# Kernel tuning notes

Measured on AMD Instinct MI355X. Metric: run time of the kernel, lower is better.

The kernel has to match this reference:

```python
import jax, jax.numpy as jnp
import numpy as np

D_MODEL = 1024
NUM_HEADS = 16
DFF = 4096
LN_EPS = 1e-08
CLIP = 10.0


def setup_inputs() -> dict:
    key = jax.random.key(0)
    ks = jax.random.split(key, 12)
    d, h, f = D_MODEL, NUM_HEADS, DFF
    s = 1.0 / np.sqrt(d)
    inp = {
        "x": jax.random.normal(ks[0], (4, 2048, d), dtype=jnp.float32),
        "wq": jax.random.normal(ks[1], (d, d), dtype=jnp.float32) * s,
        "bq": jnp.zeros((d,), jnp.float32),
        "wk": jax.random.normal(ks[2], (d, d), dtype=jnp.float32) * s,
        "bk": jnp.zeros((d,), jnp.float32),
        "wv": jax.random.normal(ks[3], (d, d), dtype=jnp.float32) * s,
        "bv": jnp.zeros((d,), jnp.float32),
        "wo": jax.random.normal(ks[4], (d, d), dtype=jnp.float32) * s,
        "bo": jnp.zeros((d,), jnp.float32),
        "w1": jax.random.normal(ks[5], (d, f), dtype=jnp.float32) * s,
        "b1": jnp.zeros((f,), jnp.float32),
        "w2": jax.random.normal(ks[6], (f, d), dtype=jnp.float32) * (1.0 / np.sqrt(f)),
        "b2": jnp.zeros((d,), jnp.float32),
        "ln_gamma": jnp.ones((d,), jnp.float32),
        "ln_beta": jnp.zeros((d,), jnp.float32),
    }
    return inp


def layernorm(x, gamma, beta):
    mu = jnp.mean(x, axis=-1, keepdims=True)
    var = jnp.var(x, axis=-1, keepdims=True)
    return (x - mu) * jax.lax.rsqrt(var + LN_EPS) * gamma + beta


def encoder_layer(x, wq, bq, wk, bk, wv, bv, wo, bo, w1, b1, w2, b2, ln_gamma, ln_beta):
    B, S, d = x.shape
    H = NUM_HEADS
    Dh = d // H
    q = (x @ wq + bq).reshape(B, S, H, Dh).transpose(0, 2, 1, 3)  # bhsd
    k = (x @ wk + bk).reshape(B, S, H, Dh).transpose(0, 2, 1, 3)
    v = (x @ wv + bv).reshape(B, S, H, Dh).transpose(0, 2, 1, 3)
    logits = jnp.einsum('bhqd,bhkd->bhqk', q, k) / jnp.sqrt(jnp.float32(Dh))
    logits = jnp.clip(logits, -CLIP, CLIP)
    attn = jax.nn.softmax(logits, axis=-1)
    ctx = jnp.einsum('bhqk,bhkd->bhqd', attn, v)
    ctx = ctx.transpose(0, 2, 1, 3).reshape(B, S, d)
    attn_out = ctx @ wo + bo
    out1 = layernorm(x + attn_out, ln_gamma, ln_beta)
    ffn = jax.nn.relu(out1 @ w1 + b1) @ w2 + b2
    return layernorm(out1 + ffn, ln_gamma, ln_beta)


def reference(x, wq, bq, wk, bk, wv, bv, wo, bo, w1, b1, w2, b2, ln_gamma, ln_beta):
    return encoder_layer(x, wq, bq, wk, bk, wv, bv, wo, bo, w1, b1, w2, b2, ln_gamma, ln_beta)
```

## Files before the change

### kernel.cpp

```cpp
#include <hip/hip_runtime.h>
#include <stdint.h>

#define D_MODEL 1024
#define NHEAD 16
#define DH 64
#define DFF 4096
#define BATCH 4
#define SEQ 2048
#define MTOT (BATCH*SEQ)

#define QSCALE 0.18033688011112043f
#define CLIP2  14.426950408889634f

typedef short short8 __attribute__((ext_vector_type(8)));
typedef float f32x4 __attribute__((ext_vector_type(4)));
typedef unsigned int uint;

__device__ inline unsigned short f2bf(float f) {
  union { float f; unsigned u; } v; v.f = f;
  unsigned r = v.u + 0x7fffu + ((v.u >> 16) & 1u);
  return (unsigned short)(r >> 16);
}
__device__ inline float bf2f(unsigned short b) {
  union { unsigned u; float f; } v; v.u = ((unsigned)b) << 16;
  return v.f;
}
__device__ inline unsigned pack_trunc(float lo, float hi) {
  union { float f; unsigned u; } a, b; a.f = lo; b.f = hi;
  return __builtin_amdgcn_perm(b.u, a.u, 0x07060302u);
}
__device__ __forceinline__ void async16(const unsigned short* g, unsigned short* l) {
  __builtin_amdgcn_global_load_lds(
      (const __attribute__((address_space(1))) unsigned int*)g,
      (__attribute__((address_space(3))) unsigned int*)l, 16, 0, 0);
}

__global__ void cast_kernel(const float* __restrict__ in, unsigned short* __restrict__ out, int n4) {
  int i = blockIdx.x * blockDim.x + threadIdx.x;
  if (i < n4) {
    float4 v = ((const float4*)in)[i];
    ushort4 o;
    o.x = f2bf(v.x); o.y = f2bf(v.y); o.z = f2bf(v.z); o.w = f2bf(v.w);
    ((ushort4*)out)[i] = o;
  }
}

__global__ void transpose_weights_kernel(
    const float* __restrict__ wq, const float* __restrict__ wk,
    const float* __restrict__ wv, const float* __restrict__ wo,
    const float* __restrict__ w1, const float* __restrict__ w2,
    unsigned short* __restrict__ wqkvT, unsigned short* __restrict__ woT,
    unsigned short* __restrict__ w1T, unsigned short* __restrict__ w2T) {
  __shared__ unsigned short tile[32][33];
  const int id = blockIdx.x;
  const float* in; unsigned short* out; int K, N, n0, k0; float scale = 1.0f;
  if (id < 4096) {
    const int wi = id >> 10, t = id & 1023;
    switch (wi) {
      case 0:  in = wq; out = wqkvT;           scale = QSCALE; break;
      case 1:  in = wk; out = wqkvT + 1048576; break;
      case 2:  in = wv; out = wqkvT + 2097152; break;
      default: in = wo; out = woT;             break;
    }
    K = 1024; N = 1024; n0 = (t & 31) * 32; k0 = (t >> 5) * 32;
  } else if (id < 8192) {
    const int t = id - 4096;
    in = w1; out = w1T; K = 1024; N = 4096; n0 = (t & 127) * 32; k0 = (t >> 7) * 32;
  } else {
    const int t = id - 8192;
    in = w2; out = w2T; K = 4096; N = 1024; n0 = (t & 31) * 32; k0 = (t >> 5) * 32;
  }
  const int tx = threadIdx.x & 31, ty = threadIdx.x >> 5;
#pragma unroll
  for (int j = 0; j < 32; j += 8)
    tile[ty + j][tx] = f2bf(in[(size_t)(k0 + ty + j) * N + n0 + tx] * scale);
  __syncthreads();
#pragma unroll
  for (int j = 0; j < 32; j += 8)
    out[(size_t)(n0 + ty + j) * K + k0 + tx] = tile[tx][ty + j];
}

__global__ void bias_concat_kernel(const float* __restrict__ bq, const float* __restrict__ bk,
                                   const float* __restrict__ bv, float* __restrict__ o) {
  int i = blockIdx.x * 256 + threadIdx.x;
  if (i < 3 * D_MODEL) {
    float v = (i < D_MODEL) ? bq[i] * QSCALE
            : (i < 2 * D_MODEL) ? bk[i - D_MODEL] : bv[i - 2 * D_MODEL];
    o[i] = v;
  }
}

__global__ void transpose_v_kernel(const unsigned short* __restrict__ QKV,
                                   unsigned short* __restrict__ Vt) {
  __shared__ unsigned short tile[32][33];
  int bh = blockIdx.z, b = bh >> 4, h = bh & 15;
  int kv0 = blockIdx.x * 32, dh0 = blockIdx.y * 32;
  int tx = threadIdx.x & 31, ty = threadIdx.x >> 5;
#pragma unroll
  for (int j = 0; j < 32; j += 8)
    tile[ty + j][tx] = QKV[(size_t)(b * SEQ + kv0 + ty + j) * 3072 + 2048 + h * DH + dh0 + tx];
  __syncthreads();
#pragma unroll
  for (int j = 0; j < 32; j += 8)
    Vt[(size_t)(bh * DH + dh0 + ty + j) * SEQ + kv0 + tx] = tile[tx][ty + j];
}

template<int RELU, int OUT_BF16, int KSPLIT, int BIAS>
__global__ __launch_bounds__(256, 4) void gemm_bt_kernel(
    const unsigned short* __restrict__ A,
    const unsigned short* __restrict__ Bt,
    const float* __restrict__ bias,
    void* __restrict__ Cout,
    int M, int N, int K) {
  __shared__ __align__(16) unsigned short As[128][32];
  __shared__ __align__(16) unsigned short Bs[128][32];
  const int GX = N >> 7;
  const int xcd = blockIdx.x & 7;
  int li = blockIdx.x >> 3;
  int kh = 0;
  if (KSPLIT == 2) { kh = li & 1; li >>= 1; }
  const int im = xcd * 8 + li / GX;
  const int in_ = li % GX;
  const int m0 = im * 128, n0 = in_ * 128;
  const int tid = threadIdx.x;
  const int wave = tid >> 6, lane = tid & 63;
  const int wm = (wave >> 1) * 64, wn = (wave & 1) * 64;
  const int lm = lane & 15, lq = lane >> 4, lk = (lane >> 4) * 8;
  const int sr = tid >> 2;
  const int sc = (tid & 3) * 8;
  f32x4 acc[4][4] = {};

  const int kbeg = (KSPLIT == 2) ? kh * (K >> 1) : 0;
  const int kend = (KSPLIT == 2) ? kbeg + (K >> 1) : K;
  for (int k0 = kbeg; k0 < kend; k0 += 32) {
    __syncthreads();
#pragma unroll
    for (int s = 0; s < 2; s++) {
      int row = sr + s * 64;
      async16(A  + (size_t)(m0 + row) * K + k0 + sc, &As[0][0] + row * 32 + sc);
      async16(Bt + (size_t)(n0 + row) * K + k0 + sc, &Bs[0][0] + row * 32 + sc);
    }
    __syncthreads();
    short8 af[4], bfr[4];
#pragma unroll
    for (int t = 0; t < 4; t++) {
      af[t]  = *(const short8*)(&As[wm + t * 16 + lm][lk]);
      bfr[t] = *(const short8*)(&Bs[wn + t * 16 + lm][lk]);
    }
#pragma unroll
    for (int mt = 0; mt < 4; mt++)
#pragma unroll
      for (int nt = 0; nt < 4; nt++)
        acc[mt][nt] = __builtin_amdgcn_mfma_f32_16x16x32_bf16(af[mt], bfr[nt], acc[mt][nt], 0, 0, 0);
  }
  unsigned short* Cb = (unsigned short*)Cout + (KSPLIT == 2 ? (size_t)kh * M * N : 0);
#pragma unroll
  for (int nt = 0; nt < 4; nt++) {
    int col = n0 + wn + nt * 16 + lm;
    float bv = BIAS ? bias[col] : 0.0f;
#pragma unroll
    for (int mt = 0; mt < 4; mt++) {
#pragma unroll
      for (int r = 0; r < 4; r++) {
        int row = m0 + wm + mt * 16 + lq * 4 + r;
        float v = acc[mt][nt][r] + bv;
        if (RELU) v = fmaxf(v, 0.0f);
        if (OUT_BF16) Cb[(size_t)row * N + col] = f2bf(v);
        else          ((float*)Cout)[(size_t)row * N + col] = v;
      }
    }
  }
}

#define MFMA_Q(mh, nh)                                                                     \
  _Pragma("unroll")                                                                        \
  for (int ks = 0; ks < 2; ks++) {                                                         \
    _Pragma("unroll")                                                                      \
    for (int i = 0; i < 4; i++) {                                                          \
      _Pragma("unroll")                                                                    \
      for (int nn = 0; nn < 2; nn++) {                                                     \
        acc[(mh)*4 + i][(nh)*2 + nn] = __builtin_amdgcn_mfma_f32_16x16x32_bf16(            \
            af[i][ks], bf[(nh)*2 + nn][ks], acc[(mh)*4 + i][(nh)*2 + nn], 0, 0, 0);        \
      }                                                                                    \
    }                                                                                      \
  }

template<int RELU, int OUT_BF16, int KSPLIT, int BIAS>
__global__ __launch_bounds__(512, 2) void gemm256_bt_kernel(
    const unsigned short* __restrict__ A,
    const unsigned short* __restrict__ Bt,
    const float* __restrict__ bias,
    void* __restrict__ Cout,
    int M, int N, int K) {
  __shared__ __align__(16) unsigned short lds[65536];

  const int nwg = gridDim.x;
  int nid = (blockIdx.x & 7) * (nwg >> 3) + (blockIdx.x >> 3);
  int kh = 0;
  if (KSPLIT == 2) { kh = nid & 1; nid >>= 1; }
  const int GX = N >> 8;
  const int im = nid / GX, in_ = nid % GX;
  const int m0 = im * 256, n0 = in_ * 256;

  const int tid = threadIdx.x;
  const int lane = tid & 63, wave = tid >> 6;
  const int wm = (wave >> 2) * 128, wn = (wave & 3) * 64;
  const int lm = lane & 15, lg = lane >> 4;
  const int rot = lm & 7;
  const int aoff0 = ((lg) ^ rot) << 3;
  const int aoff1 = ((4 + lg) ^ rot) << 3;
  const int arow = (wm + lm) << 6;
  const int brow = (wn + lm) << 6;

  const int kbeg = (KSPLIT == 2) ? kh * (K >> 1) : 0;
  const int nk = ((KSPLIT == 2) ? (K >> 1) : K) >> 6;

  const int rb = tid >> 3;
  const int gcol = (((tid & 7) ^ (rb & 7)) << 3);
  const unsigned short* gA = A  + (size_t)(m0 + rb) * K + kbeg + gcol;
  const unsigned short* gB = Bt + (size_t)(n0 + rb) * K + kbeg + gcol;

  auto stage = [&](const unsigned short* g, int b, int st, unsigned short* seg) {
    async16(g + (size_t)b * 64 * K + (size_t)st * 64, seg + b * 4096 + tid * 8);
  };

  f32x4 acc[8][4] = {};

  {
    unsigned short* A0s = lds;
    unsigned short* B0s = lds + 16384;
    unsigned short* A1s = lds + 32768;
    unsigned short* B1s = lds + 49152;
    stage(gA, 0, 0, A0s); stage(gA, 2, 0, A0s);
    stage(gB, 0, 0, B0s); stage(gB, 1, 0, B0s);
    stage(gA, 1, 0, A0s); stage(gA, 3, 0, A0s);
    stage(gB, 2, 0, B0s); stage(gB, 3, 0, B0s);
    stage(gA, 0, 1, A1s); stage(gA, 2, 1, A1s);
    stage(gB, 0, 1, B1s); stage(gB, 1, 1, B1s);
    stage(gA, 1, 1, A1s); stage(gA, 3, 1, A1s);
    __builtin_amdgcn_s_waitcnt(0x0F76);
    __builtin_amdgcn_s_barrier();
  }

  for (int t = 0; t < nk; ++t) {
    const int cur = t & 1;
    unsigned short* LA = lds + (cur << 15);
    unsigned short* LB = LA + 16384;
    unsigned short* NA = lds + ((cur ^ 1) << 15);
    unsigned short* NB = NA + 16384;
    short8 af[4][2], bf[4][2];

    if (t + 1 < nk) { stage(gB, 2, t + 1, NB); stage(gB, 3, t + 1, NB); }
#pragma unroll
    for (int i = 0; i < 4; i++) {
      af[i][0] = *(const short8*)(LA + arow + i * 1024 + aoff0);
      af[i][1] = *(const short8*)(LA + arow + i * 1024 + aoff1);
    }
#pragma unroll
    for (int n = 0; n < 2; n++) {
      bf[n][0] = *(const short8*)(LB + brow + n * 1024 + aoff0);
      bf[n][1] = *(const short8*)(LB + brow + n * 1024 + aoff1);
    }
    __builtin_amdgcn_s_barrier();
    __builtin_amdgcn_s_setprio(1);
    MFMA_Q(0, 0);
    __builtin_amdgcn_s_setprio(0);
    __builtin_amdgcn_s_barrier();

    if (t + 2 < nk) { stage(gA, 0, t + 2, LA); stage(gA, 2, t + 2, LA); }
#pragma unroll
    for (int n = 2; n < 4; n++) {
      bf[n][0] = *(const short8*)(LB + brow + n * 1024 + aoff0);
      bf[n][1] = *(const short8*)(LB + brow + n * 1024 + aoff1);
    }
    __builtin_amdgcn_s_barrier();
    __builtin_amdgcn_s_setprio(1);
    MFMA_Q(0, 1);
    __builtin_amdgcn_s_setprio(0);
    __builtin_amdgcn_s_barrier();

    if (t + 2 < nk) { stage(gB, 0, t + 2, LB); stage(gB, 1, t + 2, LB); }
#pragma unroll
    for (int i = 0; i < 4; i++) {
      af[i][0] = *(const short8*)(LA + arow + 4096 + i * 1024 + aoff0);
      af[i][1] = *(const short8*)(LA + arow + 4096 + i * 1024 + aoff1);
    }
    __builtin_amdgcn_s_barrier();
    __builtin_amdgcn_s_setprio(1);
    MFMA_Q(1, 1);
    __builtin_amdgcn_s_setprio(0);
    __builtin_amdgcn_s_barrier();

    if (t + 2 < nk) {
      stage(gA, 1, t + 2, LA); stage(gA, 3, t + 2, LA);
      __builtin_amdgcn_s_waitcnt(0x0F76);
    } else {
      __builtin_amdgcn_s_waitcnt(0x0F70);
    }
    __builtin_amdgcn_s_barrier();
    __builtin_amdgcn_s_setprio(1);
    MFMA_Q(1, 0);
    __builtin_amdgcn_s_setprio(0);
    __builtin_amdgcn_s_barrier();
  }

  unsigned short* Cb = (unsigned short*)Cout + (KSPLIT == 2 ? (size_t)kh * M * N : 0);
#pragma unroll
  for (int nt = 0; nt < 4; nt++) {
    int col = n0 + wn + nt * 16 + lm;
    float bv = BIAS ? bias[col] : 0.0f;
#pragma unroll
    for (int mf = 0; mf < 8; mf++) {
#pragma unroll
      for (int r = 0; r < 4; r++) {
        int row = m0 + wm + mf * 16 + lg * 4 + r;
        float v = acc[mf][nt][r] + bv;
        if (RELU) v = fmaxf(v, 0.0f);
        if (OUT_BF16) Cb[(size_t)row * N + col] = f2bf(v);
        else          ((float*)Cout)[(size_t)row * N + col] = v;
      }
    }
  }
}

__global__ __launch_bounds__(256, 4) void attn_kernel(
    const unsigned short* __restrict__ QKV,
    const unsigned short* __restrict__ Vt_g,
    unsigned short* __restrict__ ctx) {
  __shared__ __align__(16) unsigned short Ks[64 * 64];
  __shared__ __align__(16) unsigned short Vs[64 * 64];
  __shared__ __align__(16) unsigned short Ps[4 * 32 * 64];
  const int bh = blockIdx.x, b = bh >> 4, h = bh & 15;
  const int q0 = blockIdx.y * 128;
  const int tid = threadIdx.x, wave = tid >> 6, lane = tid & 63;
  const int lm = lane & 15, lq = lane >> 4;
  const int srow = tid >> 3, scol = (tid & 7) * 8;
  const int rot = (lm & 7) * 8;

  short8 qf[2][2];
#pragma unroll
  for (int ntq = 0; ntq < 2; ntq++) {
    const unsigned short* qp =
        QKV + (size_t)(b * SEQ + q0 + wave * 32 + ntq * 16 + lm) * 3072 + h * DH;
#pragma unroll
    for (int sl = 0; sl < 2; sl++) qf[ntq][sl] = *(const short8*)(qp + sl * 32 + lq * 8);
  }
  const short8 ones = {0x3F80, 0x3F80, 0x3F80, 0x3F80, 0x3F80, 0x3F80, 0x3F80, 0x3F80};
  f32x4 oacc[2][4] = {};
  f32x4 lsum[2] = {};

  const int sdst = srow * 64 + (scol ^ ((srow & 7) * 8));
  const unsigned short* kg = QKV + (size_t)(b * SEQ) * 3072 + D_MODEL + h * DH + scol;
  const unsigned short* vg = Vt_g + (size_t)(bh * DH + srow) * SEQ + scol;

  uint4 kr0 = *(const uint4*)(kg + (size_t)srow * 3072);
  uint4 kr1 = *(const uint4*)(kg + (size_t)(srow + 32) * 3072);
  uint4 vr0 = *(const uint4*)(vg);
  uint4 vr1 = *(const uint4*)(vg + 32 * SEQ);

  for (int it = 0; it < SEQ / 64; it++) {
    *(uint4*)(Ks + sdst)        = kr0;
    *(uint4*)(Ks + sdst + 2048) = kr1;
    *(uint4*)(Vs + sdst)        = vr0;
    *(uint4*)(Vs + sdst + 2048) = vr1;
    __syncthreads();
    if (it + 1 < SEQ / 64) {
      const int kvn = (it + 1) * 64;
      kr0 = *(const uint4*)(kg + (size_t)(kvn + srow) * 3072);
      kr1 = *(const uint4*)(kg + (size_t)(kvn + srow + 32) * 3072);
      vr0 = *(const uint4*)(vg + kvn);
      vr1 = *(const uint4*)(vg + 32 * SEQ + kvn);
    }

#pragma unroll
    for (int mt = 0; mt < 4; mt++) {
      const unsigned short* krow = Ks + (mt * 16 + lm) * 64;
      short8 kf0 = *(const short8*)(krow + ((lq * 8) ^ rot));
      short8 kf1 = *(const short8*)(krow + ((32 + lq * 8) ^ rot));
#pragma unroll
      for (int ntq = 0; ntq < 2; ntq++) {
        f32x4 sa = {0.f, 0.f, 0.f, 0.f};
        sa = __builtin_amdgcn_mfma_f32_16x16x32_bf16(kf0, qf[ntq][0], sa, 0, 0, 0);
        sa = __builtin_amdgcn_mfma_f32_16x16x32_bf16(kf1, qf[ntq][1], sa, 0, 0, 0);
        float p0 = exp2f(fminf(sa[0], CLIP2));
        float p1 = exp2f(fminf(sa[1], CLIP2));
        float p2 = exp2f(fminf(sa[2], CLIP2));
        float p3 = exp2f(fminf(sa[3], CLIP2));
        uint2 d;
        d.x = pack_trunc(p0, p1);
        d.y = pack_trunc(p2, p3);
        *(uint2*)(Ps + wave * 2048 + (ntq * 16 + lm) * 64 + ((mt * 16 + lq * 4) ^ rot)) = d;
      }
    }
    __builtin_amdgcn_s_waitcnt(0xC07F);
    short8 pf[2][2];
#pragma unroll
    for (int mq = 0; mq < 2; mq++)
#pragma unroll
      for (int sl = 0; sl < 2; sl++)
        pf[mq][sl] = *(const short8*)(Ps + wave * 2048 + (mq * 16 + lm) * 64 + ((sl * 32 + lq * 8) ^ rot));
#pragma unroll
    for (int nt = 0; nt < 4; nt++) {
      const unsigned short* vrow = Vs + (nt * 16 + lm) * 64;
      short8 vf0 = *(const short8*)(vrow + ((lq * 8) ^ rot));
      short8 vf1 = *(const short8*)(vrow + ((32 + lq * 8) ^ rot));
#pragma unroll
      for (int mq = 0; mq < 2; mq++) {
        oacc[mq][nt] = __builtin_amdgcn_mfma_f32_16x16x32_bf16(pf[mq][0], vf0, oacc[mq][nt], 0, 0, 0);
        oacc[mq][nt] = __builtin_amdgcn_mfma_f32_16x16x32_bf16(pf[mq][1], vf1, oacc[mq][nt], 0, 0, 0);
      }
    }
#pragma unroll
    for (int mq = 0; mq < 2; mq++) {
      lsum[mq] = __builtin_amdgcn_mfma_f32_16x16x32_bf16(pf[mq][0], ones, lsum[mq], 0, 0, 0);
      lsum[mq] = __builtin_amdgcn_mfma_f32_16x16x32_bf16(pf[mq][1], ones, lsum[mq], 0, 0, 0);
    }
    __syncthreads();
  }

#pragma unroll
  for (int mq = 0; mq < 2; mq++) {
    float linv[4];
#pragma unroll
    for (int r = 0; r < 4; r++) linv[r] = 1.0f / lsum[mq][r];
    const size_t rowbase =
        (size_t)(b * SEQ + q0 + wave * 32 + mq * 16 + lq * 4) * D_MODEL + h * DH;
#pragma unroll
    for (int nt = 0; nt < 4; nt++) {
#pragma unroll
      for (int r = 0; r < 4; r++) {
        ctx[rowbase + (size_t)r * D_MODEL + nt * 16 + lm] = f2bf(oacc[mq][nt][r] * linv[r]);
      }
    }
  }
}

template<int B_BF16, int WRITE_BF16, int THREE>
__global__ void ln_kernel(const float* __restrict__ A, const void* __restrict__ Bv,
                          const void* __restrict__ B2v, const float* __restrict__ cbias,
                          const float* __restrict__ gamma, const float* __restrict__ beta,
                          float* __restrict__ outf, unsigned short* __restrict__ outb) {
  const int row = blockIdx.x;
  const int tid = threadIdx.x;
  const size_t base = (size_t)row * D_MODEL + tid * 4;
  float4 xa = *(const float4*)(A + base);
  float4 xb;
  if (B_BF16) {
    ushort4 u = *(const ushort4*)((const unsigned short*)Bv + base);
    xb.x = bf2f(u.x); xb.y = bf2f(u.y); xb.z = bf2f(u.z); xb.w = bf2f(u.w);
  } else {
    xb = *(const float4*)((const float*)Bv + base);
  }
  if (THREE) {
    ushort4 u2 = *(const ushort4*)((const unsigned short*)B2v + base);
    float4 cb = *(const float4*)(cbias + tid * 4);
    xb.x += bf2f(u2.x) + cb.x; xb.y += bf2f(u2.y) + cb.y;
    xb.z += bf2f(u2.z) + cb.z; xb.w += bf2f(u2.w) + cb.w;
  }
  float v0 = xa.x + xb.x, v1 = xa.y + xb.y, v2 = xa.z + xb.z, v3 = xa.w + xb.w;
  float s = v0 + v1 + v2 + v3;
  float sq = v0 * v0 + v1 * v1 + v2 * v2 + v3 * v3;
#pragma unroll
  for (int off = 1; off < 64; off <<= 1) {
    s  += __shfl_xor(s, off);
    sq += __shfl_xor(sq, off);
  }
  __shared__ float red[8];
  int wave = tid >> 6;
  if ((tid & 63) == 0) { red[wave * 2] = s; red[wave * 2 + 1] = sq; }
  __syncthreads();
  s  = red[0] + red[2] + red[4] + red[6];
  sq = red[1] + red[3] + red[5] + red[7];
  float mean = s * (1.0f / D_MODEL);
  float var = sq * (1.0f / D_MODEL) - mean * mean;
  float inv = rsqrtf(var + 1e-8f);
  float4 g  = *(const float4*)(gamma + tid * 4);
  float4 be = *(const float4*)(beta + tid * 4);
  float o0 = (v0 - mean) * inv * g.x + be.x;
  float o1 = (v1 - mean) * inv * g.y + be.y;
  float o2 = (v2 - mean) * inv * g.z + be.z;
  float o3 = (v3 - mean) * inv * g.w + be.w;
  float4 of; of.x = o0; of.y = o1; of.z = o2; of.w = o3;
  *(float4*)(outf + base) = of;
  if (WRITE_BF16) {
    ushort4 ub; ub.x = f2bf(o0); ub.y = f2bf(o1); ub.z = f2bf(o2); ub.w = f2bf(o3);
    *(ushort4*)(outb + base) = ub;
  }
}

extern "C" void kernel_launch(void* const* d_in, const int* in_sizes, int n_in,
                              void* d_out, int out_size, void* d_ws, size_t ws_size,
                              hipStream_t stream) {
  const float* x     = (const float*)d_in[0];
  const float* wq    = (const float*)d_in[1];
  const float* bq    = (const float*)d_in[2];
  const float* wk    = (const float*)d_in[3];
  const float* bk    = (const float*)d_in[4];
  const float* wv    = (const float*)d_in[5];
  const float* bv    = (const float*)d_in[6];
  const float* wo    = (const float*)d_in[7];
  const float* bo    = (const float*)d_in[8];
  const float* w1    = (const float*)d_in[9];
  const float* b1    = (const float*)d_in[10];
  const float* w2    = (const float*)d_in[11];
  const float* b2    = (const float*)d_in[12];
  const float* gamma = (const float*)d_in[13];
  const float* beta  = (const float*)d_in[14];

  char* ws = (char*)d_ws;
  const size_t MB = 1ull << 20;
  unsigned short* xb      = (unsigned short*)(ws + 0 * MB);
  unsigned short* out1b   = (unsigned short*)(ws + 0 * MB);
  unsigned short* ffn2    = (unsigned short*)(ws + 0 * MB);
  unsigned short* wqkvT   = (unsigned short*)(ws + 16 * MB);
  unsigned short* woT     = (unsigned short*)(ws + 22 * MB);
  unsigned short* w1T     = (unsigned short*)(ws + 24 * MB);
  unsigned short* w2T     = (unsigned short*)(ws + 32 * MB);
  float*          bqkv    = (float*)(ws + 40 * MB);
  unsigned short* qkvb    = (unsigned short*)(ws + 41 * MB);
  unsigned short* attnoutb= (unsigned short*)(ws + 41 * MB);
  unsigned short* h1      = (unsigned short*)(ws + 41 * MB);
  unsigned short* Vt_g    = (unsigned short*)(ws + 89 * MB);
  unsigned short* ctx     = (unsigned short*)(ws + 105 * MB);
  float*          out1f   = (float*)(ws + 121 * MB);

  cast_kernel<<<(MTOT * D_MODEL / 4 + 255) / 256, 256, 0, stream>>>(x, xb, MTOT * D_MODEL / 4);
  transpose_weights_kernel<<<12288, 256, 0, stream>>>(
      wq, wk, wv, wo, w1, w2, wqkvT, woT, w1T, w2T);
  bias_concat_kernel<<<12, 256, 0, stream>>>(bq, bk, bv, bqkv);

  gemm256_bt_kernel<0, 1, 1, 1><<<(3072 / 256) * (MTOT / 256), 512, 0, stream>>>(
      xb, wqkvT, bqkv, qkvb, MTOT, 3072, D_MODEL);
  transpose_v_kernel<<<dim3(SEQ / 32, DH / 32, BATCH * NHEAD), 256, 0, stream>>>(qkvb, Vt_g);
  attn_kernel<<<dim3(BATCH * NHEAD, SEQ / 128), 256, 0, stream>>>(qkvb, Vt_g, ctx);

  gemm_bt_kernel<0, 1, 1, 1><<<(D_MODEL / 128) * (MTOT / 128), 256, 0, stream>>>(
      ctx, woT, bo, attnoutb, MTOT, D_MODEL, D_MODEL);
  ln_kernel<1, 1, 0><<<MTOT, 256, 0, stream>>>(
      x, attnoutb, nullptr, nullptr, gamma, beta, out1f, out1b);
  gemm256_bt_kernel<1, 1, 1, 1><<<(DFF / 256) * (MTOT / 256), 512, 0, stream>>>(
      out1b, w1T, b1, h1, MTOT, DFF, D_MODEL);
  gemm256_bt_kernel<0, 1, 2, 0><<<2 * (D_MODEL / 256) * (MTOT / 256), 512, 0, stream>>>(
      h1, w2T, nullptr, ffn2, MTOT, D_MODEL, DFF);
  ln_kernel<1, 0, 1><<<MTOT, 256, 0, stream>>>(
      out1f, ffn2, ffn2 + (size_t)MTOT * D_MODEL, b2, gamma, beta, (float*)d_out, nullptr);
}
```

Baseline: 543.4 us.

## Double-buffer attention K/V with async loads, widen weight transpose, split-K out-proj

The attention kernel now uses 512 threads covering 256 queries. K/V tiles are double-buffered through async global-to-LDS copies, with one barrier per iteration and s_setprio around the MFMA sections. The weight-transpose kernel moves to 64x64 tiles with float4 reads and 16-byte writes. The output projection switches to the 256-tile GEMM with split-K, and the two partial sums plus bias are folded into the LayerNorm. The aim is to hide K/V load latency, cut barrier overhead and improve GEMM efficiency, at the cost of more LDS, an extra partial buffer and an added reduction in the LN.

```diff
diff --git a/kernel.cpp b/kernel.cpp
--- a/kernel.cpp
+++ b/kernel.cpp
@@ -51,33 +51,40 @@
     const float* __restrict__ w1, const float* __restrict__ w2,
     unsigned short* __restrict__ wqkvT, unsigned short* __restrict__ woT,
     unsigned short* __restrict__ w1T, unsigned short* __restrict__ w2T) {
-  __shared__ unsigned short tile[32][33];
+  __shared__ __align__(16) unsigned short tile[64][72];
   const int id = blockIdx.x;
   const float* in; unsigned short* out; int K, N, n0, k0; float scale = 1.0f;
-  if (id < 4096) {
-    const int wi = id >> 10, t = id & 1023;
+  if (id < 1024) {
+    const int wi = id >> 8, t = id & 255;
     switch (wi) {
       case 0:  in = wq; out = wqkvT;           scale = QSCALE; break;
       case 1:  in = wk; out = wqkvT + 1048576; break;
       case 2:  in = wv; out = wqkvT + 2097152; break;
       default: in = wo; out = woT;             break;
     }
-    K = 1024; N = 1024; n0 = (t & 31) * 32; k0 = (t >> 5) * 32;
-  } else if (id < 8192) {
-    const int t = id - 4096;
-    in = w1; out = w1T; K = 1024; N = 4096; n0 = (t & 127) * 32; k0 = (t >> 7) * 32;
+    K = 1024; N = 1024; n0 = (t & 15) * 64; k0 = (t >> 4) * 64;
+  } else if (id < 2048) {
+    const int t = id - 1024;
+    in = w1; out = w1T; K = 1024; N = 4096; n0 = (t & 63) * 64; k0 = (t >> 6) * 64;
   } else {
-    const int t = id - 8192;
-    in = w2; out = w2T; K = 4096; N = 1024; n0 = (t & 31) * 32; k0 = (t >> 5) * 32;
-  }
-  const int tx = threadIdx.x & 31, ty = threadIdx.x >> 5;
-#pragma unroll
-  for (int j = 0; j < 32; j += 8)
-    tile[ty + j][tx] = f2bf(in[(size_t)(k0 + ty + j) * N + n0 + tx] * scale);
+    const int t = id - 2048;
+    in = w2; out = w2T; K = 4096; N = 1024; n0 = (t & 15) * 64; k0 = (t >> 4) * 64;
+  }
+  const int tx = threadIdx.x & 15, ty = threadIdx.x >> 4;
+#pragma unroll
+  for (int j = 0; j < 64; j += 16) {
+    float4 v = *(const float4*)(in + (size_t)(k0 + ty + j) * N + n0 + tx * 4);
+    tile[tx * 4 + 0][ty + j] = f2bf(v.x * scale);
+    tile[tx * 4 + 1][ty + j] = f2bf(v.y * scale);
+    tile[tx * 4 + 2][ty + j] = f2bf(v.z * scale);
+    tile[tx * 4 + 3][ty + j] = f2bf(v.w * scale);
+  }
   __syncthreads();
-#pragma unroll
-  for (int j = 0; j < 32; j += 8)
-    out[(size_t)(n0 + ty + j) * K + k0 + tx] = tile[tx][ty + j];
+  const int r = threadIdx.x >> 3, c = threadIdx.x & 7;
+#pragma unroll
+  for (int j = 0; j < 64; j += 32)
+    *(uint4*)(out + (size_t)(n0 + r + j) * K + k0 + c * 8) =
+        *(const uint4*)(&tile[r + j][c * 8]);
 }
 
 __global__ void bias_concat_kernel(const float* __restrict__ bq, const float* __restrict__ bk,
@@ -103,73 +110,6 @@
 #pragma unroll
   for (int j = 0; j < 32; j += 8)
     Vt[(size_t)(bh * DH + dh0 + ty + j) * SEQ + kv0 + tx] = tile[tx][ty + j];
-}
-
-template<int RELU, int OUT_BF16, int KSPLIT, int BIAS>
-__global__ __launch_bounds__(256, 4) void gemm_bt_kernel(
-    const unsigned short* __restrict__ A,
-    const unsigned short* __restrict__ Bt,
-    const float* __restrict__ bias,
-    void* __restrict__ Cout,
-    int M, int N, int K) {
-  __shared__ __align__(16) unsigned short As[128][32];
-  __shared__ __align__(16) unsigned short Bs[128][32];
-  const int GX = N >> 7;
-  const int xcd = blockIdx.x & 7;
-  int li = blockIdx.x >> 3;
-  int kh = 0;
-  if (KSPLIT == 2) { kh = li & 1; li >>= 1; }
-  const int im = xcd * 8 + li / GX;
-  const int in_ = li % GX;
-  const int m0 = im * 128, n0 = in_ * 128;
-  const int tid = threadIdx.x;
-  const int wave = tid >> 6, lane = tid & 63;
-  const int wm = (wave >> 1) * 64, wn = (wave & 1) * 64;
-  const int lm = lane & 15, lq = lane >> 4, lk = (lane >> 4) * 8;
-  const int sr = tid >> 2;
-  const int sc = (tid & 3) * 8;
-  f32x4 acc[4][4] = {};
-
-  const int kbeg = (KSPLIT == 2) ? kh * (K >> 1) : 0;
-  const int kend = (KSPLIT == 2) ? kbeg + (K >> 1) : K;
-  for (int k0 = kbeg; k0 < kend; k0 += 32) {
-    __syncthreads();
-#pragma unroll
-    for (int s = 0; s < 2; s++) {
-      int row = sr + s * 64;
-      async16(A  + (size_t)(m0 + row) * K + k0 + sc, &As[0][0] + row * 32 + sc);
-      async16(Bt + (size_t)(n0 + row) * K + k0 + sc, &Bs[0][0] + row * 32 + sc);
-    }
-    __syncthreads();
-    short8 af[4], bfr[4];
-#pragma unroll
-    for (int t = 0; t < 4; t++) {
-      af[t]  = *(const short8*)(&As[wm + t * 16 + lm][lk]);
-      bfr[t] = *(const short8*)(&Bs[wn + t * 16 + lm][lk]);
-    }
-#pragma unroll
-    for (int mt = 0; mt < 4; mt++)
-#pragma unroll
-      for (int nt = 0; nt < 4; nt++)
-        acc[mt][nt] = __builtin_amdgcn_mfma_f32_16x16x32_bf16(af[mt], bfr[nt], acc[mt][nt], 0, 0, 0);
-  }
-  unsigned short* Cb = (unsigned short*)Cout + (KSPLIT == 2 ? (size_t)kh * M * N : 0);
-#pragma unroll
-  for (int nt = 0; nt < 4; nt++) {
-    int col = n0 + wn + nt * 16 + lm;
-    float bv = BIAS ? bias[col] : 0.0f;
-#pragma unroll
-    for (int mt = 0; mt < 4; mt++) {
-#pragma unroll
-      for (int r = 0; r < 4; r++) {
-        int row = m0 + wm + mt * 16 + lq * 4 + r;
-        float v = acc[mt][nt][r] + bv;
-        if (RELU) v = fmaxf(v, 0.0f);
-        if (OUT_BF16) Cb[(size_t)row * N + col] = f2bf(v);
-        else          ((float*)Cout)[(size_t)row * N + col] = v;
-      }
-    }
-  }
 }
 
 #define MFMA_Q(mh, nh)                                                                     \
@@ -323,18 +263,17 @@
   }
 }
 
-__global__ __launch_bounds__(256, 4) void attn_kernel(
+__global__ __launch_bounds__(512, 4) void attn_kernel(
     const unsigned short* __restrict__ QKV,
     const unsigned short* __restrict__ Vt_g,
     unsigned short* __restrict__ ctx) {
-  __shared__ __align__(16) unsigned short Ks[64 * 64];
-  __shared__ __align__(16) unsigned short Vs[64 * 64];
-  __shared__ __align__(16) unsigned short Ps[4 * 32 * 64];
+  __shared__ __align__(16) unsigned short Ks[2][4096];
+  __shared__ __align__(16) unsigned short Vs[2][4096];
+  __shared__ __align__(16) unsigned short Ps[8 * 2048];
   const int bh = blockIdx.x, b = bh >> 4, h = bh & 15;
-  const int q0 = blockIdx.y * 128;
+  const int q0 = blockIdx.y * 256;
   const int tid = threadIdx.x, wave = tid >> 6, lane = tid & 63;
   const int lm = lane & 15, lq = lane >> 4;
-  const int srow = tid >> 3, scol = (tid & 7) * 8;
   const int rot = (lm & 7) * 8;
 
   short8 qf[2][2];
@@ -349,39 +288,42 @@
   f32x4 oacc[2][4] = {};
   f32x4 lsum[2] = {};
 
-  const int sdst = srow * 64 + (scol ^ ((srow & 7) * 8));
-  const unsigned short* kg = QKV + (size_t)(b * SEQ) * 3072 + D_MODEL + h * DH + scol;
-  const unsigned short* vg = Vt_g + (size_t)(bh * DH + srow) * SEQ + scol;
-
-  uint4 kr0 = *(const uint4*)(kg + (size_t)srow * 3072);
-  uint4 kr1 = *(const uint4*)(kg + (size_t)(srow + 32) * 3072);
-  uint4 vr0 = *(const uint4*)(vg);
-  uint4 vr1 = *(const uint4*)(vg + 32 * SEQ);
+  const int srow = tid >> 3;
+  const int ssl = (tid & 7) ^ (srow & 7);
+  const unsigned short* kg =
+      QKV + (size_t)(b * SEQ + srow) * 3072 + D_MODEL + h * DH + ssl * 8;
+  const unsigned short* vg = Vt_g + (size_t)(bh * DH + srow) * SEQ + ssl * 8;
+  unsigned short* kdst = &Ks[0][0] + tid * 8;
+  unsigned short* vdst = &Vs[0][0] + tid * 8;
+
+  async16(kg, kdst);
+  async16(vg, vdst);
 
   for (int it = 0; it < SEQ / 64; it++) {
-    *(uint4*)(Ks + sdst)        = kr0;
-    *(uint4*)(Ks + sdst + 2048) = kr1;
-    *(uint4*)(Vs + sdst)        = vr0;
-    *(uint4*)(Vs + sdst + 2048) = vr1;
-    __syncthreads();
+    const int buf = it & 1;
+    __builtin_amdgcn_s_waitcnt(0x0F70);
+    __builtin_amdgcn_s_barrier();
+    __builtin_amdgcn_sched_barrier(0);
     if (it + 1 < SEQ / 64) {
-      const int kvn = (it + 1) * 64;
-      kr0 = *(const uint4*)(kg + (size_t)(kvn + srow) * 3072);
-      kr1 = *(const uint4*)(kg + (size_t)(kvn + srow + 32) * 3072);
-      vr0 = *(const uint4*)(vg + kvn);
-      vr1 = *(const uint4*)(vg + 32 * SEQ + kvn);
-    }
+      const int nb = (buf ^ 1) * 4096;
+      async16(kg + (size_t)(it + 1) * 64 * 3072, kdst + nb);
+      async16(vg + (it + 1) * 64, vdst + nb);
+    }
+    const unsigned short* Kb = &Ks[buf][0];
+    const unsigned short* Vb = &Vs[buf][0];
 
 #pragma unroll
     for (int mt = 0; mt < 4; mt++) {
-      const unsigned short* krow = Ks + (mt * 16 + lm) * 64;
+      const unsigned short* krow = Kb + (mt * 16 + lm) * 64;
       short8 kf0 = *(const short8*)(krow + ((lq * 8) ^ rot));
       short8 kf1 = *(const short8*)(krow + ((32 + lq * 8) ^ rot));
 #pragma unroll
       for (int ntq = 0; ntq < 2; ntq++) {
         f32x4 sa = {0.f, 0.f, 0.f, 0.f};
+        __builtin_amdgcn_s_setprio(1);
         sa = __builtin_amdgcn_mfma_f32_16x16x32_bf16(kf0, qf[ntq][0], sa, 0, 0, 0);
         sa = __builtin_amdgcn_mfma_f32_16x16x32_bf16(kf1, qf[ntq][1], sa, 0, 0, 0);
+        __builtin_amdgcn_s_setprio(0);
         float p0 = exp2f(fminf(sa[0], CLIP2));
         float p1 = exp2f(fminf(sa[1], CLIP2));
         float p2 = exp2f(fminf(sa[2], CLIP2));
@@ -399,9 +341,10 @@
 #pragma unroll
       for (int sl = 0; sl < 2; sl++)
         pf[mq][sl] = *(const short8*)(Ps + wave * 2048 + (mq * 16 + lm) * 64 + ((sl * 32 + lq * 8) ^ rot));
+    __builtin_amdgcn_s_setprio(1);
 #pragma unroll
     for (int nt = 0; nt < 4; nt++) {
-      const unsigned short* vrow = Vs + (nt * 16 + lm) * 64;
+      const unsigned short* vrow = Vb + (nt * 16 + lm) * 64;
       short8 vf0 = *(const short8*)(vrow + ((lq * 8) ^ rot));
       short8 vf1 = *(const short8*)(vrow + ((32 + lq * 8) ^ rot));
 #pragma unroll
@@ -415,7 +358,7 @@
       lsum[mq] = __builtin_amdgcn_mfma_f32_16x16x32_bf16(pf[mq][0], ones, lsum[mq], 0, 0, 0);
       lsum[mq] = __builtin_amdgcn_mfma_f32_16x16x32_bf16(pf[mq][1], ones, lsum[mq], 0, 0, 0);
     }
-    __syncthreads();
+    __builtin_amdgcn_s_setprio(0);
   }
 
 #pragma unroll
@@ -518,26 +461,26 @@
   unsigned short* w2T     = (unsigned short*)(ws + 32 * MB);
   float*          bqkv    = (float*)(ws + 40 * MB);
   unsigned short* qkvb    = (unsigned short*)(ws + 41 * MB);
-  unsigned short* attnoutb= (unsigned short*)(ws + 41 * MB);
+  unsigned short* oprojp  = (unsigned short*)(ws + 41 * MB);
   unsigned short* h1      = (unsigned short*)(ws + 41 * MB);
   unsigned short* Vt_g    = (unsigned short*)(ws + 89 * MB);
   unsigned short* ctx     = (unsigned short*)(ws + 105 * MB);
   float*          out1f   = (float*)(ws + 121 * MB);
 
   cast_kernel<<<(MTOT * D_MODEL / 4 + 255) / 256, 256, 0, stream>>>(x, xb, MTOT * D_MODEL / 4);
-  transpose_weights_kernel<<<12288, 256, 0, stream>>>(
+  transpose_weights_kernel<<<3072, 256, 0, stream>>>(
       wq, wk, wv, wo, w1, w2, wqkvT, woT, w1T, w2T);
   bias_concat_kernel<<<12, 256, 0, stream>>>(bq, bk, bv, bqkv);
 
   gemm256_bt_kernel<0, 1, 1, 1><<<(3072 / 256) * (MTOT / 256), 512, 0, stream>>>(
       xb, wqkvT, bqkv, qkvb, MTOT, 3072, D_MODEL);
   transpose_v_kernel<<<dim3(SEQ / 32, DH / 32, BATCH * NHEAD), 256, 0, stream>>>(qkvb, Vt_g);
-  attn_kernel<<<dim3(BATCH * NHEAD, SEQ / 128), 256, 0, stream>>>(qkvb, Vt_g, ctx);
-
-  gemm_bt_kernel<0, 1, 1, 1><<<(D_MODEL / 128) * (MTOT / 128), 256, 0, stream>>>(
-      ctx, woT, bo, attnoutb, MTOT, D_MODEL, D_MODEL);
-  ln_kernel<1, 1, 0><<<MTOT, 256, 0, stream>>>(
-      x, attnoutb, nullptr, nullptr, gamma, beta, out1f, out1b);
+  attn_kernel<<<dim3(BATCH * NHEAD, SEQ / 256), 512, 0, stream>>>(qkvb, Vt_g, ctx);
+
+  gemm256_bt_kernel<0, 1, 2, 0><<<2 * (D_MODEL / 256) * (MTOT / 256), 512, 0, stream>>>(
+      ctx, woT, nullptr, oprojp, MTOT, D_MODEL, D_MODEL);
+  ln_kernel<1, 1, 1><<<MTOT, 256, 0, stream>>>(
+      x, oprojp, oprojp + (size_t)MTOT * D_MODEL, bo, gamma, beta, out1f, out1b);
   gemm256_bt_kernel<1, 1, 1, 1><<<(DFF / 256) * (MTOT / 256), 512, 0, stream>>>(
       out1b, w1T, b1, h1, MTOT, DFF, D_MODEL);
   gemm256_bt_kernel<0, 1, 2, 0><<<2 * (D_MODEL / 256) * (MTOT / 256), 512, 0, stream>>>(
```

Result: no change. 541.5 us (-0.4%).
